# Optimization experiments

Hardware: AMD Instinct MI355X
Metric: run time of the kernel (lower is better)

Reference implementation:

```python
import jax, jax.numpy as jnp
import numpy as np
from jax import lax

NUM_CLASSES = 9
IMG_H, IMG_W = 384, 640
SCORE_TH = 0.05
NMS_TH = 0.5
DET_PER_IMG = 100
PRE_NMS_K = 512  # pre-NMS top-k candidates per image (fixed-shape surrogate for nonzero())
BBOX_XFORM_CLIP = float(np.log(1000.0 / 16.0))
WX, WY, WW, WH = 10.0, 10.0, 5.0, 5.0
MIN_SIZE = 0.01


def _conv(x, w, padding):
    return lax.conv_general_dilated(x, w, (1, 1), padding,
                                    dimension_numbers=('NCHW', 'OIHW', 'NCHW'))


def _pairwise_iou(a, b):
    # a [K,4], b [K,4] -> [K,K]
    area_a = (a[:, 2] - a[:, 0]) * (a[:, 3] - a[:, 1])
    area_b = (b[:, 2] - b[:, 0]) * (b[:, 3] - b[:, 1])
    lt = jnp.maximum(a[:, None, :2], b[None, :, :2])
    rb = jnp.minimum(a[:, None, 2:], b[None, :, 2:])
    wh = jnp.clip(rb - lt, 0.0)
    inter = wh[..., 0] * wh[..., 1]
    return inter / jnp.maximum(area_a[:, None] + area_b[None, :] - inter, 1e-8)


def setup_inputs() -> dict:
    key = jax.random.key(0)
    ks = jax.random.split(key, 12)
    B, P, C_in = 2, 512, 512
    feats = jax.random.normal(ks[0], (B * P, C_in, 7, 7), jnp.float32)
    # well-formed proposal boxes inside the image
    cx = jax.random.uniform(ks[1], (B, P)) * IMG_W
    cy = jax.random.uniform(ks[2], (B, P)) * IMG_H
    w = jax.random.uniform(ks[3], (B, P)) * 100.0 + 8.0
    h = jax.random.uniform(ks[4], (B, P)) * 100.0 + 8.0
    proposals = jnp.stack([cx - w / 2, cy - h / 2, cx + w / 2, cy + h / 2], -1)
    w1 = jax.random.normal(ks[5], (1024, C_in, 3, 3), jnp.float32) * 0.02
    w2 = jax.random.normal(ks[6], (1024, 1024, 3, 3), jnp.float32) * 0.02
    wd = jax.random.normal(ks[7], (1024, C_in, 1, 1), jnp.float32) * 0.02
    cls_w = jax.random.normal(ks[8], (NUM_CLASSES, 1024), jnp.float32) * 0.02
    cls_b = jnp.zeros((NUM_CLASSES,), jnp.float32)
    reg_w = jax.random.normal(ks[9], (NUM_CLASSES * 4, 1024), jnp.float32) * 0.02
    reg_b = jnp.zeros((NUM_CLASSES * 4,), jnp.float32)
    return dict(instance_features=feats, proposals=proposals, w1=w1, w2=w2, wd=wd,
                cls_w=cls_w, cls_b=cls_b, reg_w=reg_w, reg_b=reg_b)


def _per_image(boxes, scores):
    # boxes [P, C, 4], scores [P, C]
    P = boxes.shape[0]
    b = boxes[:, 1:].reshape(-1, 4)                 # drop background class
    s = scores[:, 1:].reshape(-1)
    lab = jnp.broadcast_to(jnp.arange(1, NUM_CLASSES), (P, NUM_CLASSES - 1)).reshape(-1)
    ws = b[:, 2] - b[:, 0]
    hs = b[:, 3] - b[:, 1]
    valid = (s > SCORE_TH) & (ws >= MIN_SIZE) & (hs >= MIN_SIZE)
    s = jnp.where(valid, s, -jnp.inf)
    s_top, idx = lax.top_k(s, PRE_NMS_K)            # sorted descending -> greedy NMS order
    b_top = b[idx]
    lab_top = lab[idx]
    # class-aware NMS via per-class coordinate offset (batched_nms trick)
    off = lab_top.astype(b.dtype)[:, None] * (float(max(IMG_H, IMG_W)) + 1.0)
    iou = _pairwise_iou(b_top + off, b_top + off)
    keep0 = jnp.isfinite(s_top)
    ar = jnp.arange(PRE_NMS_K)

    def body(i, keep):
        sup = (iou[i] > NMS_TH) & (ar > i) & keep[i]
        return keep & ~sup

    keep = lax.fori_loop(0, PRE_NMS_K, body, keep0)
    ks = jnp.where(keep, s_top, -jnp.inf)
    fs, fidx = lax.top_k(ks, DET_PER_IMG)
    fb = b_top[fidx]
    fl = lab_top[fidx]
    fvalid = jnp.isfinite(fs)
    return (jnp.where(fvalid[:, None], fb, 0.0),
            jnp.where(fvalid, fs, 0.0),
            jnp.where(fvalid, fl, 0),
            fvalid)


def reference(instance_features, proposals, w1, w2, wd, cls_w, cls_b, reg_w, reg_b):
    B, P = proposals.shape[0], proposals.shape[1]
    x = instance_features
    # Residual_Basic: two 3x3 convs + 1x1 downsample shortcut, relu
    h = jax.nn.relu(_conv(x, w1, 'SAME'))
    h = _conv(h, w2, 'SAME')
    embedded = jax.nn.relu(h + _conv(x, wd, 'VALID'))          # [N,1024,7,7]
    flat = embedded.mean(axis=(2, 3))                          # AdaptiveAvgPool2d(1)+Flatten
    cls_scores = flat @ cls_w.T + cls_b                        # [N, C]
    bbox_reg = flat @ reg_w.T + reg_b                          # [N, 4C]

    # ---- box decode (BoxCoder weights (10,10,5,5)) ----
    props = proposals.reshape(-1, 4)
    pw = props[:, 2] - props[:, 0]
    ph = props[:, 3] - props[:, 1]
    pcx = props[:, 0] + 0.5 * pw
    pcy = props[:, 1] + 0.5 * ph
    rel = bbox_reg.reshape(-1, NUM_CLASSES, 4)
    dx = rel[..., 0] / WX
    dy = rel[..., 1] / WY
    dw = jnp.minimum(rel[..., 2] / WW, BBOX_XFORM_CLIP)
    dh = jnp.minimum(rel[..., 3] / WH, BBOX_XFORM_CLIP)
    ncx = dx * pw[:, None] + pcx[:, None]
    ncy = dy * ph[:, None] + pcy[:, None]
    nw = jnp.exp(dw) * pw[:, None]
    nh = jnp.exp(dh) * ph[:, None]
    pred_boxes = jnp.stack([ncx - 0.5 * nw, ncy - 0.5 * nh,
                            ncx + 0.5 * nw, ncy + 0.5 * nh], -1)  # [N,C,4]
    # clip to image
    pred_boxes = jnp.stack([
        jnp.clip(pred_boxes[..., 0], 0.0, IMG_W),
        jnp.clip(pred_boxes[..., 1], 0.0, IMG_H),
        jnp.clip(pred_boxes[..., 2], 0.0, IMG_W),
        jnp.clip(pred_boxes[..., 3], 0.0, IMG_H)], -1)
    pred_scores = jax.nn.softmax(cls_scores, -1)

    det_boxes, det_scores, det_labels, det_valid = jax.vmap(_per_image)(
        pred_boxes.reshape(B, P, NUM_CLASSES, 4),
        pred_scores.reshape(B, P, NUM_CLASSES))
    return embedded, cls_scores, bbox_reg, det_boxes, det_scores, det_labels, det_valid
```

## Files before the change

### kernel.cpp

```cpp
#include <hip/hip_runtime.h>
#include <math.h>

#define N_IMG 1024
#define C_IN 512
#define C_MID 1024
#define HW 7
#define SP 49
#define NCOLS (N_IMG*SP)
#define LDSROW 40
#define AROW 32

typedef short bf16x8 __attribute__((ext_vector_type(8)));
typedef float f32x4  __attribute__((ext_vector_type(4)));

__device__ __forceinline__ void dma16(const void* g, void* l) {
    __builtin_amdgcn_global_load_lds(
        (const __attribute__((address_space(1))) void*)g,
        (__attribute__((address_space(3))) void*)l, 16, 0, 0);
}

__device__ __forceinline__ unsigned splitpack(float v) {
    unsigned u  = __float_as_uint(v);
    unsigned hi = (u + 0x7FFFu + ((u >> 16) & 1u)) >> 16;
    float hf    = __uint_as_float(hi << 16);
    float d     = v - hf;
    unsigned ud = __float_as_uint(d);
    unsigned lo = (ud + 0x7FFFu + ((ud >> 16) & 1u)) >> 16;
    return (hi & 0xFFFFu) | (lo << 16);
}

__global__ __launch_bounds__(256)
void pack_x(const float* __restrict__ X, unsigned* __restrict__ Xpk)
{
    int i = blockIdx.x*256 + threadIdx.x;
    Xpk[i] = splitpack(X[i]);
}

__global__ __launch_bounds__(256)
void pack_w1(const float* __restrict__ w, unsigned short* __restrict__ Wh,
             unsigned short* __restrict__ Wl)
{
    int e = blockIdx.x*256 + threadIdx.x;
    int cp = e & 31, oc = (e>>5)&127, bm = (e>>12)&7, cc = (e>>15)&15, r = e>>19;
    float v = w[((size_t)(bm*128+oc)*512 + (cc*32+cp))*9 + r];
    unsigned pk = splitpack(v);
    Wh[e] = (unsigned short)(pk & 0xFFFFu);
    Wl[e] = (unsigned short)(pk >> 16);
}
__global__ __launch_bounds__(256)
void pack_w2(const float* __restrict__ w, unsigned short* __restrict__ Wh,
             unsigned short* __restrict__ Wl)
{
    int e = blockIdx.x*256 + threadIdx.x;
    int cp = e & 31, oc = (e>>5)&127, bm = (e>>12)&7, cc = (e>>15)&31, r = e>>20;
    float v = w[((size_t)(bm*128+oc)*1024 + (cc*32+cp))*9 + r];
    unsigned pk = splitpack(v);
    Wh[e] = (unsigned short)(pk & 0xFFFFu);
    Wl[e] = (unsigned short)(pk >> 16);
}
__global__ __launch_bounds__(256)
void pack_wd(const float* __restrict__ w, unsigned short* __restrict__ Wh,
             unsigned short* __restrict__ Wl)
{
    int e = blockIdx.x*256 + threadIdx.x;
    int cp = e & 31, oc = (e>>5)&127, bm = (e>>12)&7, cc = e>>15;
    float v = w[(size_t)(bm*128+oc)*512 + cc*32+cp];
    unsigned pk = splitpack(v);
    Wh[e] = (unsigned short)(pk & 0xFFFFu);
    Wl[e] = (unsigned short)(pk >> 16);
}

template<int MODE>
__global__ __launch_bounds__(256)
void conv_mfma(const unsigned* __restrict__ Bpk,
               const float* __restrict__ Xf,
               const unsigned short* __restrict__ Wh,
               const unsigned short* __restrict__ Wl,
               const unsigned short* __restrict__ Dh,
               const unsigned short* __restrict__ Dl,
               float* __restrict__ outF, unsigned* __restrict__ outU)
{
    constexpr int CS  = MODE ? C_MID : C_IN;
    constexpr int NCC = MODE ? 32 : 16;
    __shared__ __align__(16) unsigned short As_hi[128*AROW];
    __shared__ __align__(16) unsigned short As_lo[128*AROW];
    __shared__ __align__(16) unsigned short Bs_hi[128*LDSROW];
    __shared__ __align__(16) unsigned short Bs_lo[128*LDSROW];

    const int tid = threadIdx.x;
    const int bid  = blockIdx.x;
    const int xcd  = bid & 7;
    const int slot = bid >> 3;
    const int bm   = slot & 7;
    const int bn   = xcd*49 + (slot >> 3);

    const int ln = tid & 63;
    const int wv = tid >> 6;
    const int lm = ln & 15, lq = ln >> 4;
    const int wm = (wv & 1) * 64;
    const int wn = (wv >> 1) * 64;
    const int koff = lq * 8;

    const int go = wv*1024 + ln*8;

    const int bcol = tid >> 1;
    const int half16 = (tid & 1) * 16;
    const int col = bn*128 + bcol;
    const int bnimg = col / SP;
    const int bp = col - bnimg*SP;
    const int by = bp / HW;
    const int bx = bp - by*HW;
    const int bo = bcol*LDSROW + half16;

    f32x4 acc[4][4];
    #pragma unroll
    for (int i = 0; i < 4; i++)
        #pragma unroll
        for (int j = 0; j < 4; j++)
            acc[i][j] = (f32x4){0.f, 0.f, 0.f, 0.f};

    for (int cc = 0; cc < NCC; ++cc) {
        const unsigned* srcb = Bpk + ((size_t)bnimg*CS + cc*32 + half16)*SP;
        for (int r = 0; r < 9; ++r) {
            const int t3 = r / 3;
            const int dy = t3 - 1;
            const int dx = (r - t3*3) - 1;
            const bool valid = ((unsigned)(by + dy) < (unsigned)HW) &&
                               ((unsigned)(bx + dx) < (unsigned)HW);
            const int pp = bp + dy*HW + dx;
            {
                const size_t tb = ((size_t)((r*NCC + cc)*8 + bm) << 12);
                dma16(Wh + tb + go,       &As_hi[wv*1024]);
                dma16(Wh + tb + go + 512, &As_hi[wv*1024 + 512]);
                dma16(Wl + tb + go,       &As_lo[wv*1024]);
                dma16(Wl + tb + go + 512, &As_lo[wv*1024 + 512]);
            }
            {
                unsigned v[16];
                if (valid) {
                    const unsigned* src = srcb + pp;
                    #pragma unroll
                    for (int e = 0; e < 16; ++e) v[e] = src[e*SP];
                } else {
                    #pragma unroll
                    for (int e = 0; e < 16; ++e) v[e] = 0u;
                }
                unsigned hp[8], lp[8];
                #pragma unroll
                for (int j2 = 0; j2 < 8; ++j2) {
                    unsigned p0 = v[2*j2], p1 = v[2*j2+1];
                    hp[j2] = (p0 & 0xFFFFu) | (p1 << 16);
                    lp[j2] = (p0 >> 16) | (p1 & 0xFFFF0000u);
                }
                *(uint4*)&Bs_hi[bo]     = *(uint4*)&hp[0];
                *(uint4*)&Bs_hi[bo + 8] = *(uint4*)&hp[4];
                *(uint4*)&Bs_lo[bo]     = *(uint4*)&lp[0];
                *(uint4*)&Bs_lo[bo + 8] = *(uint4*)&lp[4];
            }
            __syncthreads();
            {
                bf16x8 ah[4], bh[4], al[4], bl[4];
                #pragma unroll
                for (int i = 0; i < 4; i++)
                    ah[i] = *(const bf16x8*)&As_hi[(wm + i*16 + lm)*AROW + koff];
                #pragma unroll
                for (int j = 0; j < 4; j++)
                    bh[j] = *(const bf16x8*)&Bs_hi[(wn + j*16 + lm)*LDSROW + koff];
                #pragma unroll
                for (int i = 0; i < 4; i++)
                    #pragma unroll
                    for (int j = 0; j < 4; j++)
                        acc[i][j] = __builtin_amdgcn_mfma_f32_16x16x32_bf16(
                            ah[i], bh[j], acc[i][j], 0, 0, 0);
                #pragma unroll
                for (int i = 0; i < 4; i++)
                    al[i] = *(const bf16x8*)&As_lo[(wm + i*16 + lm)*AROW + koff];
                #pragma unroll
                for (int i = 0; i < 4; i++)
                    #pragma unroll
                    for (int j = 0; j < 4; j++)
                        acc[i][j] = __builtin_amdgcn_mfma_f32_16x16x32_bf16(
                            al[i], bh[j], acc[i][j], 0, 0, 0);
                #pragma unroll
                for (int j = 0; j < 4; j++)
                    bl[j] = *(const bf16x8*)&Bs_lo[(wn + j*16 + lm)*LDSROW + koff];
                #pragma unroll
                for (int i = 0; i < 4; i++)
                    #pragma unroll
                    for (int j = 0; j < 4; j++)
                        acc[i][j] = __builtin_amdgcn_mfma_f32_16x16x32_bf16(
                            ah[i], bl[j], acc[i][j], 0, 0, 0);
            }
            __syncthreads();
        }
    }
    if (MODE == 1) {
        for (int cc = 0; cc < 16; ++cc) {
            {
                const size_t tb = ((size_t)(cc*8 + bm) << 12);
                dma16(Dh + tb + go,       &As_hi[wv*1024]);
                dma16(Dh + tb + go + 512, &As_hi[wv*1024 + 512]);
                dma16(Dl + tb + go,       &As_lo[wv*1024]);
                dma16(Dl + tb + go + 512, &As_lo[wv*1024 + 512]);
            }
            {
                const float* src = Xf + ((size_t)bnimg*C_IN + cc*32 + half16)*SP + bp;
                unsigned v[16];
                #pragma unroll
                for (int e = 0; e < 16; ++e) v[e] = splitpack(src[e*SP]);
                unsigned hp[8], lp[8];
                #pragma unroll
                for (int j2 = 0; j2 < 8; ++j2) {
                    unsigned p0 = v[2*j2], p1 = v[2*j2+1];
                    hp[j2] = (p0 & 0xFFFFu) | (p1 << 16);
                    lp[j2] = (p0 >> 16) | (p1 & 0xFFFF0000u);
                }
                *(uint4*)&Bs_hi[bo]     = *(uint4*)&hp[0];
                *(uint4*)&Bs_hi[bo + 8] = *(uint4*)&hp[4];
                *(uint4*)&Bs_lo[bo]     = *(uint4*)&lp[0];
                *(uint4*)&Bs_lo[bo + 8] = *(uint4*)&lp[4];
            }
            __syncthreads();
            {
                bf16x8 ah[4], bh[4], al[4], bl[4];
                #pragma unroll
                for (int i = 0; i < 4; i++)
                    ah[i] = *(const bf16x8*)&As_hi[(wm + i*16 + lm)*AROW + koff];
                #pragma unroll
                for (int j = 0; j < 4; j++)
                    bh[j] = *(const bf16x8*)&Bs_hi[(wn + j*16 + lm)*LDSROW + koff];
                #pragma unroll
                for (int i = 0; i < 4; i++)
                    #pragma unroll
                    for (int j = 0; j < 4; j++)
                        acc[i][j] = __builtin_amdgcn_mfma_f32_16x16x32_bf16(
                            ah[i], bh[j], acc[i][j], 0, 0, 0);
                #pragma unroll
                for (int i = 0; i < 4; i++)
                    al[i] = *(const bf16x8*)&As_lo[(wm + i*16 + lm)*AROW + koff];
                #pragma unroll
                for (int i = 0; i < 4; i++)
                    #pragma unroll
                    for (int j = 0; j < 4; j++)
                        acc[i][j] = __builtin_amdgcn_mfma_f32_16x16x32_bf16(
                            al[i], bh[j], acc[i][j], 0, 0, 0);
                #pragma unroll
                for (int j = 0; j < 4; j++)
                    bl[j] = *(const bf16x8*)&Bs_lo[(wn + j*16 + lm)*LDSROW + koff];
                #pragma unroll
                for (int i = 0; i < 4; i++)
                    #pragma unroll
                    for (int j = 0; j < 4; j++)
                        acc[i][j] = __builtin_amdgcn_mfma_f32_16x16x32_bf16(
                            ah[i], bl[j], acc[i][j], 0, 0, 0);
            }
            __syncthreads();
        }
    }

    #pragma unroll
    for (int j = 0; j < 4; j++) {
        const int gc = bn*128 + wn + j*16 + lm;
        const int n = gc / SP;
        const int p = gc - n*SP;
        #pragma unroll
        for (int i = 0; i < 4; i++) {
            #pragma unroll
            for (int r = 0; r < 4; r++) {
                const int m = bm*128 + wm + i*16 + lq*4 + r;
                float val = fmaxf(acc[i][j][r], 0.f);
                if (MODE == 0)
                    outU[((size_t)n*C_MID + m)*SP + p] = splitpack(val);
                else
                    outF[((size_t)n*C_MID + m)*SP + p] = val;
            }
        }
    }
}

__global__ __launch_bounds__(256)
void pool_kernel(const float* __restrict__ emb, float* __restrict__ flat)
{
    int n = blockIdx.x;
    for (int c = threadIdx.x; c < C_MID; c += 256) {
        const float* p = emb + ((size_t)n*C_MID + c)*SP;
        float s = 0.f;
        #pragma unroll
        for (int i = 0; i < SP; i++) s += p[i];
        flat[n*C_MID + c] = s / 49.0f;
    }
}

__global__ __launch_bounds__(64)
void head_kernel(const float* __restrict__ flat,
                 const float* __restrict__ cls_w, const float* __restrict__ cls_b,
                 const float* __restrict__ reg_w, const float* __restrict__ reg_b,
                 const float* __restrict__ props,
                 float* __restrict__ cls_out, float* __restrict__ reg_out,
                 float* __restrict__ pbox, float* __restrict__ pscore)
{
    int n = blockIdx.x;
    __shared__ float f[C_MID];
    __shared__ float logits[9];
    __shared__ float regs[36];
    for (int c = threadIdx.x; c < C_MID; c += 64) f[c] = flat[n*C_MID + c];
    __syncthreads();
    int o = threadIdx.x;
    if (o < 45) {
        const float* w = (o < 9) ? (cls_w + o*C_MID) : (reg_w + (o-9)*C_MID);
        float a = (o < 9) ? cls_b[o] : reg_b[o-9];
        for (int c = 0; c < C_MID; c++) a = fmaf(f[c], w[c], a);
        if (o < 9) { cls_out[n*9 + o] = a; logits[o] = a; }
        else       { reg_out[n*36 + (o-9)] = a; regs[o-9] = a; }
    }
    __syncthreads();
    if (o < 9) {
        float m = logits[0];
        for (int i = 1; i < 9; i++) m = fmaxf(m, logits[i]);
        float se = 0.f;
        for (int i = 0; i < 9; i++) se += expf(logits[i] - m);
        pscore[n*9 + o] = expf(logits[o] - m) / se;
        {
            #pragma clang fp contract(off)
            float x1 = props[n*4+0], y1 = props[n*4+1];
            float x2 = props[n*4+2], y2 = props[n*4+3];
            float pw = x2 - x1, ph = y2 - y1;
            float pcx = x1 + 0.5f*pw, pcy = y1 + 0.5f*ph;
            float dx = regs[o*4+0] / 10.0f;
            float dy = regs[o*4+1] / 10.0f;
            float dw = fminf(regs[o*4+2] / 5.0f, 4.135166556742356f);
            float dh = fminf(regs[o*4+3] / 5.0f, 4.135166556742356f);
            float ncx = dx*pw + pcx, ncy = dy*ph + pcy;
            float nw = expf(dw)*pw,  nh = expf(dh)*ph;
            float bx1 = ncx - 0.5f*nw, by1 = ncy - 0.5f*nh;
            float bx2 = ncx + 0.5f*nw, by2 = ncy + 0.5f*nh;
            bx1 = fminf(fmaxf(bx1, 0.f), 640.f);
            by1 = fminf(fmaxf(by1, 0.f), 384.f);
            bx2 = fminf(fmaxf(bx2, 0.f), 640.f);
            by2 = fminf(fmaxf(by2, 0.f), 384.f);
            float* dst = pbox + (n*9 + o)*4;
            dst[0] = bx1; dst[1] = by1; dst[2] = bx2; dst[3] = by2;
        }
    }
}

__global__ __launch_bounds__(1024)
void nms_kernel(const float* __restrict__ pbox, const float* __restrict__ pscore,
                float* __restrict__ dbox, float* __restrict__ dsc,
                float* __restrict__ dlab, float* __restrict__ dval)
{
    #pragma clang fp contract(off)
    const int b = blockIdx.x;
    const int tid = threadIdx.x;
    __shared__ unsigned long long mbuf[4096];
    __shared__ float s512[512];
    __shared__ int   id512[512];
    __shared__ float obx[512][4];
    __shared__ unsigned long long keepw[8];
    float* sc = (float*)mbuf;
    int*   si = (int*)(sc + 4096);
    const float NEG_INF = -__builtin_inff();

    for (int i = tid; i < 4096; i += 1024) {
        int p = i >> 3;
        int c = (i & 7) + 1;
        int n = b*512 + p;
        float s = pscore[n*9 + c];
        const float* bb = pbox + (n*9 + c)*4;
        float w = bb[2] - bb[0], h = bb[3] - bb[1];
        bool valid = (s > 0.05f) && (w >= 0.01f) && (h >= 0.01f);
        sc[i] = valid ? s : NEG_INF;
        si[i] = i;
    }
    __syncthreads();
    for (int k = 2; k <= 4096; k <<= 1) {
        for (int j = k >> 1; j > 0; j >>= 1) {
            for (int i = tid; i < 4096; i += 1024) {
                int ixj = i ^ j;
                if (ixj > i) {
                    float s1 = sc[i], s2 = sc[ixj];
                    int i1 = si[i], i2 = si[ixj];
                    bool before12 = (s1 > s2) || ((s1 == s2) && (i1 < i2));
                    bool up = ((i & k) == 0);
                    if (up ? !before12 : before12) {
                        sc[i] = s2; sc[ixj] = s1;
                        si[i] = i2; si[ixj] = i1;
                    }
                }
            }
            __syncthreads();
        }
    }
    if (tid < 512) {
        float s = sc[tid];
        int id = si[tid];
        s512[tid] = s;
        id512[tid] = id;
        int c = (id & 7) + 1;
        int n = b*512 + (id >> 3);
        float off = (float)c * 641.0f;
        const float* bb = pbox + (n*9 + c)*4;
        obx[tid][0] = bb[0] + off;
        obx[tid][1] = bb[1] + off;
        obx[tid][2] = bb[2] + off;
        obx[tid][3] = bb[3] + off;
    }
    __syncthreads();
    unsigned long long* mask = mbuf;
    for (int idx = tid; idx < 4096; idx += 1024) {
        int i = idx >> 3, w = idx & 7;
        float ax1 = obx[i][0], ay1 = obx[i][1], ax2 = obx[i][2], ay2 = obx[i][3];
        float aarea = (ax2 - ax1) * (ay2 - ay1);
        unsigned long long m = 0;
        int j0 = w << 6;
        for (int jj = 0; jj < 64; jj++) {
            int j = j0 + jj;
            if (j > i) {
                float bx1 = obx[j][0], by1 = obx[j][1];
                float bx2 = obx[j][2], by2 = obx[j][3];
                float barea = (bx2 - bx1) * (by2 - by1);
                float lx = fmaxf(ax1, bx1), ly = fmaxf(ay1, by1);
                float rx = fminf(ax2, bx2), ry = fminf(ay2, by2);
                float iw = fmaxf(rx - lx, 0.f), ih = fmaxf(ry - ly, 0.f);
                float inter = iw * ih;
                float iou = inter / fmaxf(aarea + barea - inter, 1e-8f);
                if (iou > 0.5f) m |= (1ull << jj);
            }
        }
        mask[(i << 3) + w] = m;
    }
    if (tid < 8) {
        unsigned long long kw = 0;
        for (int jj = 0; jj < 64; jj++)
            if (s512[(tid << 6) + jj] != NEG_INF) kw |= (1ull << jj);
        keepw[tid] = kw;
    }
    __syncthreads();
    if (tid == 0) {
        for (int i = 0; i < 512; i++) {
            if ((keepw[i >> 6] >> (i & 63)) & 1ull) {
                const unsigned long long* mi = mask + (i << 3);
                #pragma unroll
                for (int w = 0; w < 8; w++) keepw[w] &= ~mi[w];
            }
        }
        int cnt = 0;
        for (int i = 0; i < 512 && cnt < 100; i++) {
            if ((keepw[i >> 6] >> (i & 63)) & 1ull) {
                int id = id512[i];
                int c = (id & 7) + 1;
                int n = b*512 + (id >> 3);
                const float* bb = pbox + (n*9 + c)*4;
                float* db = dbox + (b*100 + cnt)*4;
                db[0] = bb[0]; db[1] = bb[1]; db[2] = bb[2]; db[3] = bb[3];
                dsc[b*100 + cnt] = s512[i];
                dlab[b*100 + cnt] = (float)c;
                dval[b*100 + cnt] = 1.0f;
                cnt++;
            }
        }
        for (; cnt < 100; cnt++) {
            float* db = dbox + (b*100 + cnt)*4;
            db[0] = 0.f; db[1] = 0.f; db[2] = 0.f; db[3] = 0.f;
            dsc[b*100 + cnt] = 0.f;
            dlab[b*100 + cnt] = 0.f;
            dval[b*100 + cnt] = 0.f;
        }
    }
}

extern "C" void kernel_launch(void* const* d_in, const int* in_sizes, int n_in,
                              void* d_out, int out_size, void* d_ws, size_t ws_size,
                              hipStream_t stream)
{
    const float* X      = (const float*)d_in[0];
    const float* props  = (const float*)d_in[1];
    const float* w1     = (const float*)d_in[2];
    const float* w2     = (const float*)d_in[3];
    const float* wd     = (const float*)d_in[4];
    const float* cls_w  = (const float*)d_in[5];
    const float* cls_b  = (const float*)d_in[6];
    const float* reg_w  = (const float*)d_in[7];
    const float* reg_b  = (const float*)d_in[8];

    float* out     = (float*)d_out;
    float* emb     = out;
    float* cls_out = out + 51380224;
    float* reg_out = cls_out + 9216;
    float* dbox    = reg_out + 36864;
    float* dsc     = dbox + 800;
    float* dlab    = dsc + 200;
    float* dval    = dlab + 200;

    unsigned* Xpk            = (unsigned*)out;
    unsigned short* Wpk1h    = (unsigned short*)(out + 25690112);
    unsigned short* Wpk1l    = (unsigned short*)(out + 30408704);

    char* wsb = (char*)d_ws;
    unsigned* h_u         = (unsigned*)(wsb);
    unsigned short* Wpk2h = (unsigned short*)(wsb + 205520896);
    unsigned short* Wpk2l = (unsigned short*)(wsb + 224395264);
    unsigned short* Wpkdh = (unsigned short*)(wsb + 243269632);
    unsigned short* Wpkdl = (unsigned short*)(wsb + 244318208);
    float* flat           = (float*)(wsb + 245366784);
    float* pbox           = (float*)(wsb + 249561088);
    float* pscore         = (float*)(wsb + 249708544);

    pack_x <<<100352, 256, 0, stream>>>(X, Xpk);
    pack_w1<<<18432,  256, 0, stream>>>(w1, Wpk1h, Wpk1l);
    pack_w2<<<36864,  256, 0, stream>>>(w2, Wpk2h, Wpk2l);
    pack_wd<<<2048,   256, 0, stream>>>(wd, Wpkdh, Wpkdl);

    conv_mfma<0><<<3136, 256, 0, stream>>>(Xpk, X, Wpk1h, Wpk1l,
                                           nullptr, nullptr, nullptr, h_u);
    conv_mfma<1><<<3136, 256, 0, stream>>>(h_u, X, Wpk2h, Wpk2l,
                                           Wpkdh, Wpkdl, emb, nullptr);
    pool_kernel<<<N_IMG, 256, 0, stream>>>(emb, flat);
    head_kernel<<<N_IMG, 64, 0, stream>>>(flat, cls_w, cls_b, reg_w, reg_b, props,
                                          cls_out, reg_out, pbox, pscore);
    nms_kernel<<<2, 1024, 0, stream>>>(pbox, pscore, dbox, dsc, dlab, dval);
}
```

Before: 5.194 ms.

## Double-buffer LDS tiles and prefetch next K-step during MFMA compute

Merges the 3x3 conv loop and the downsample loop into one flattened tile sequence and double-buffers the A and B shared-memory tiles. The next tile's weight DMA and activation global loads are issued before computing the current tile, and the B tile is written to LDS afterward, which cuts one barrier per step and hides load latency behind MFMA work. The cost is twice the LDS footprint (which may lower occupancy), extra registers for the prefetched values, and a per-step branch selecting the source.

```diff
diff --git a/kernel.cpp b/kernel.cpp
--- a/kernel.cpp
+++ b/kernel.cpp
@@ -82,10 +82,14 @@
 {
     constexpr int CS  = MODE ? C_MID : C_IN;
     constexpr int NCC = MODE ? 32 : 16;
-    __shared__ __align__(16) unsigned short As_hi[128*AROW];
-    __shared__ __align__(16) unsigned short As_lo[128*AROW];
-    __shared__ __align__(16) unsigned short Bs_hi[128*LDSROW];
-    __shared__ __align__(16) unsigned short Bs_lo[128*LDSROW];
+    constexpr int NT_MAIN = NCC * 9;
+    constexpr int NT = MODE ? (NT_MAIN + 16) : NT_MAIN;
+    constexpr int AHALF = 128*AROW;
+    constexpr int BHALF = 128*LDSROW;
+    __shared__ __align__(16) unsigned short As_hi[2*AHALF];
+    __shared__ __align__(16) unsigned short As_lo[2*AHALF];
+    __shared__ __align__(16) unsigned short Bs_hi[2*BHALF];
+    __shared__ __align__(16) unsigned short Bs_lo[2*BHALF];
 
     const int tid = threadIdx.x;
     const int bid  = blockIdx.x;
@@ -119,143 +123,130 @@
         for (int j = 0; j < 4; j++)
             acc[i][j] = (f32x4){0.f, 0.f, 0.f, 0.f};
 
-    for (int cc = 0; cc < NCC; ++cc) {
-        const unsigned* srcb = Bpk + ((size_t)bnimg*CS + cc*32 + half16)*SP;
-        for (int r = 0; r < 9; ++r) {
+    auto a_dma = [&](int t, int pb) {
+        const unsigned short* sh;
+        const unsigned short* sl;
+        size_t tb;
+        if (MODE == 1 && t >= NT_MAIN) {
+            const int cc = t - NT_MAIN;
+            tb = ((size_t)(cc*8 + bm) << 12);
+            sh = Dh; sl = Dl;
+        } else {
+            const int cc = t/9, r = t - cc*9;
+            tb = ((size_t)((r*NCC + cc)*8 + bm) << 12);
+            sh = Wh; sl = Wl;
+        }
+        unsigned short* dh = &As_hi[pb*AHALF + wv*1024];
+        unsigned short* dl = &As_lo[pb*AHALF + wv*1024];
+        dma16(sh + tb + go,       dh);
+        dma16(sh + tb + go + 512, dh + 512);
+        dma16(sl + tb + go,       dl);
+        dma16(sl + tb + go + 512, dl + 512);
+    };
+
+    auto b_load = [&](int t, unsigned* v) {
+        if (MODE == 1 && t >= NT_MAIN) {
+            const int cc = t - NT_MAIN;
+            const unsigned* src = (const unsigned*)
+                (Xf + ((size_t)bnimg*C_IN + cc*32 + half16)*SP + bp);
+            #pragma unroll
+            for (int e = 0; e < 16; ++e) v[e] = src[e*SP];
+        } else {
+            const int cc = t/9, r = t - cc*9;
             const int t3 = r / 3;
             const int dy = t3 - 1;
             const int dx = (r - t3*3) - 1;
             const bool valid = ((unsigned)(by + dy) < (unsigned)HW) &&
                                ((unsigned)(bx + dx) < (unsigned)HW);
-            const int pp = bp + dy*HW + dx;
-            {
-                const size_t tb = ((size_t)((r*NCC + cc)*8 + bm) << 12);
-                dma16(Wh + tb + go,       &As_hi[wv*1024]);
-                dma16(Wh + tb + go + 512, &As_hi[wv*1024 + 512]);
-                dma16(Wl + tb + go,       &As_lo[wv*1024]);
-                dma16(Wl + tb + go + 512, &As_lo[wv*1024 + 512]);
+            const unsigned* src =
+                Bpk + ((size_t)bnimg*CS + cc*32 + half16)*SP + (bp + dy*HW + dx);
+            if (valid) {
+                #pragma unroll
+                for (int e = 0; e < 16; ++e) v[e] = src[e*SP];
+            } else {
+                #pragma unroll
+                for (int e = 0; e < 16; ++e) v[e] = 0u;
             }
-            {
-                unsigned v[16];
-                if (valid) {
-                    const unsigned* src = srcb + pp;
-                    #pragma unroll
-                    for (int e = 0; e < 16; ++e) v[e] = src[e*SP];
-                } else {
-                    #pragma unroll
-                    for (int e = 0; e < 16; ++e) v[e] = 0u;
-                }
-                unsigned hp[8], lp[8];
-                #pragma unroll
-                for (int j2 = 0; j2 < 8; ++j2) {
-                    unsigned p0 = v[2*j2], p1 = v[2*j2+1];
-                    hp[j2] = (p0 & 0xFFFFu) | (p1 << 16);
-                    lp[j2] = (p0 >> 16) | (p1 & 0xFFFF0000u);
-                }
-                *(uint4*)&Bs_hi[bo]     = *(uint4*)&hp[0];
-                *(uint4*)&Bs_hi[bo + 8] = *(uint4*)&hp[4];
-                *(uint4*)&Bs_lo[bo]     = *(uint4*)&lp[0];
-                *(uint4*)&Bs_lo[bo + 8] = *(uint4*)&lp[4];
-            }
-            __syncthreads();
-            {
-                bf16x8 ah[4], bh[4], al[4], bl[4];
-                #pragma unroll
-                for (int i = 0; i < 4; i++)
-                    ah[i] = *(const bf16x8*)&As_hi[(wm + i*16 + lm)*AROW + koff];
-                #pragma unroll
-                for (int j = 0; j < 4; j++)
-                    bh[j] = *(const bf16x8*)&Bs_hi[(wn + j*16 + lm)*LDSROW + koff];
-                #pragma unroll
-                for (int i = 0; i < 4; i++)
-                    #pragma unroll
-                    for (int j = 0; j < 4; j++)
-                        acc[i][j] = __builtin_amdgcn_mfma_f32_16x16x32_bf16(
-                            ah[i], bh[j], acc[i][j], 0, 0, 0);
-                #pragma unroll
-                for (int i = 0; i < 4; i++)
-                    al[i] = *(const bf16x8*)&As_lo[(wm + i*16 + lm)*AROW + koff];
-                #pragma unroll
-                for (int i = 0; i < 4; i++)
-                    #pragma unroll
-                    for (int j = 0; j < 4; j++)
-                        acc[i][j] = __builtin_amdgcn_mfma_f32_16x16x32_bf16(
-                            al[i], bh[j], acc[i][j], 0, 0, 0);
-                #pragma unroll
-                for (int j = 0; j < 4; j++)
-                    bl[j] = *(const bf16x8*)&Bs_lo[(wn + j*16 + lm)*LDSROW + koff];
-                #pragma unroll
-                for (int i = 0; i < 4; i++)
-                    #pragma unroll
-                    for (int j = 0; j < 4; j++)
-                        acc[i][j] = __builtin_amdgcn_mfma_f32_16x16x32_bf16(
-                            ah[i], bl[j], acc[i][j], 0, 0, 0);
-            }
-            __syncthreads();
-        }
-    }
-    if (MODE == 1) {
-        for (int cc = 0; cc < 16; ++cc) {
-            {
-                const size_t tb = ((size_t)(cc*8 + bm) << 12);
-                dma16(Dh + tb + go,       &As_hi[wv*1024]);
-                dma16(Dh + tb + go + 512, &As_hi[wv*1024 + 512]);
-                dma16(Dl + tb + go,       &As_lo[wv*1024]);
-                dma16(Dl + tb + go + 512, &As_lo[wv*1024 + 512]);
-            }
-            {
-                const float* src = Xf + ((size_t)bnimg*C_IN + cc*32 + half16)*SP + bp;
-                unsigned v[16];
-                #pragma unroll
-                for (int e = 0; e < 16; ++e) v[e] = splitpack(src[e*SP]);
-                unsigned hp[8], lp[8];
-                #pragma unroll
-                for (int j2 = 0; j2 < 8; ++j2) {
-                    unsigned p0 = v[2*j2], p1 = v[2*j2+1];
-                    hp[j2] = (p0 & 0xFFFFu) | (p1 << 16);
-                    lp[j2] = (p0 >> 16) | (p1 & 0xFFFF0000u);
-                }
-                *(uint4*)&Bs_hi[bo]     = *(uint4*)&hp[0];
-                *(uint4*)&Bs_hi[bo + 8] = *(uint4*)&hp[4];
-                *(uint4*)&Bs_lo[bo]     = *(uint4*)&lp[0];
-                *(uint4*)&Bs_lo[bo + 8] = *(uint4*)&lp[4];
-            }
-            __syncthreads();
-            {
-                bf16x8 ah[4], bh[4], al[4], bl[4];
-                #pragma unroll
-                for (int i = 0; i < 4; i++)
-                    ah[i] = *(const bf16x8*)&As_hi[(wm + i*16 + lm)*AROW + koff];
-                #pragma unroll
-                for (int j = 0; j < 4; j++)
-                    bh[j] = *(const bf16x8*)&Bs_hi[(wn + j*16 + lm)*LDSROW + koff];
-                #pragma unroll
-                for (int i = 0; i < 4; i++)
-                    #pragma unroll
-                    for (int j = 0; j < 4; j++)
-                        acc[i][j] = __builtin_amdgcn_mfma_f32_16x16x32_bf16(
-                            ah[i], bh[j], acc[i][j], 0, 0, 0);
-                #pragma unroll
-                for (int i = 0; i < 4; i++)
-                    al[i] = *(const bf16x8*)&As_lo[(wm + i*16 + lm)*AROW + koff];
-                #pragma unroll
-                for (int i = 0; i < 4; i++)
-                    #pragma unroll
-                    for (int j = 0; j < 4; j++)
-                        acc[i][j] = __builtin_amdgcn_mfma_f32_16x16x32_bf16(
-                            al[i], bh[j], acc[i][j], 0, 0, 0);
-                #pragma unroll
-                for (int j = 0; j < 4; j++)
-                    bl[j] = *(const bf16x8*)&Bs_lo[(wn + j*16 + lm)*LDSROW + koff];
-                #pragma unroll
-                for (int i = 0; i < 4; i++)
-                    #pragma unroll
-                    for (int j = 0; j < 4; j++)
-                        acc[i][j] = __builtin_amdgcn_mfma_f32_16x16x32_bf16(
-                            ah[i], bl[j], acc[i][j], 0, 0, 0);
-            }
-            __syncthreads();
-        }
+        }
+    };
+
+    auto b_write = [&](int t, unsigned* v, int pb) {
+        if (MODE == 1 && t >= NT_MAIN) {
+            #pragma unroll
+            for (int e = 0; e < 16; ++e) v[e] = splitpack(__uint_as_float(v[e]));
+        }
+        unsigned hp[8], lp[8];
+        #pragma unroll
+        for (int j2 = 0; j2 < 8; ++j2) {
+            unsigned p0 = v[2*j2], p1 = v[2*j2+1];
+            hp[j2] = (p0 & 0xFFFFu) | (p1 << 16);
+            lp[j2] = (p0 >> 16) | (p1 & 0xFFFF0000u);
+        }
+        const int o = pb*BHALF + bo;
+        *(uint4*)&Bs_hi[o]     = *(uint4*)&hp[0];
+        *(uint4*)&Bs_hi[o + 8] = *(uint4*)&hp[4];
+        *(uint4*)&Bs_lo[o]     = *(uint4*)&lp[0];
+        *(uint4*)&Bs_lo[o + 8] = *(uint4*)&lp[4];
+    };
+
+    auto compute = [&](int pb) {
+        const unsigned short* Ah = &As_hi[pb*AHALF];
+        const unsigned short* Al = &As_lo[pb*AHALF];
+        const unsigned short* Bh = &Bs_hi[pb*BHALF];
+        const unsigned short* Bl = &Bs_lo[pb*BHALF];
+        bf16x8 ah[4], bh[4], al[4], bl[4];
+        #pragma unroll
+        for (int i = 0; i < 4; i++)
+            ah[i] = *(const bf16x8*)&Ah[(wm + i*16 + lm)*AROW + koff];
+        #pragma unroll
+        for (int j = 0; j < 4; j++)
+            bh[j] = *(const bf16x8*)&Bh[(wn + j*16 + lm)*LDSROW + koff];
+        #pragma unroll
+        for (int i = 0; i < 4; i++)
+            #pragma unroll
+            for (int j = 0; j < 4; j++)
+                acc[i][j] = __builtin_amdgcn_mfma_f32_16x16x32_bf16(
+                    ah[i], bh[j], acc[i][j], 0, 0, 0);
+        #pragma unroll
+        for (int i = 0; i < 4; i++)
+            al[i] = *(const bf16x8*)&Al[(wm + i*16 + lm)*AROW + koff];
+        #pragma unroll
+        for (int i = 0; i < 4; i++)
+            #pragma unroll
+            for (int j = 0; j < 4; j++)
+                acc[i][j] = __builtin_amdgcn_mfma_f32_16x16x32_bf16(
+                    al[i], bh[j], acc[i][j], 0, 0, 0);
+        #pragma unroll
+        for (int j = 0; j < 4; j++)
+            bl[j] = *(const bf16x8*)&Bl[(wn + j*16 + lm)*LDSROW + koff];
+        #pragma unroll
+        for (int i = 0; i < 4; i++)
+            #pragma unroll
+            for (int j = 0; j < 4; j++)
+                acc[i][j] = __builtin_amdgcn_mfma_f32_16x16x32_bf16(
+                    ah[i], bl[j], acc[i][j], 0, 0, 0);
+    };
+
+    {
+        unsigned v[16];
+        b_load(0, v);
+        a_dma(0, 0);
+        b_write(0, v, 0);
+    }
+    __syncthreads();
+    int pb = 0;
+    for (int t = 0; t < NT; ++t) {
+        unsigned vn[16];
+        const bool more = (t + 1 < NT);
+        if (more) {
+            b_load(t + 1, vn);
+            a_dma(t + 1, pb ^ 1);
+        }
+        compute(pb);
+        if (more)
+            b_write(t + 1, vn, pb ^ 1);
+        __syncthreads();
+        pb ^= 1;
     }
 
     #pragma unroll
```

Result: slower. 7.107 ms (+36.8%).
